# Optimization experiments

Measured on AMD Instinct MI355X. Metric: run time of the kernel, lower is better.

The kernel has to match this reference:

```python
import jax, jax.numpy as jnp
import numpy as np

EPS = 1e-3  # keras LayerNormalization default epsilon

def _ln(x, gamma, beta):
    m = jnp.mean(x, axis=-1, keepdims=True)
    v = jnp.var(x, axis=-1, keepdims=True)
    return gamma * (x - m) * jax.lax.rsqrt(v + EPS) + beta

def setup_inputs() -> dict:
    B, T, F, H = 256, 128, 4, 512  # T*F must equal H (skip-connection constraint in context GRN)
    D = T * F
    key = jax.random.key(0)
    ks = jax.random.split(key, 16)
    s = lambda fan: 1.0 / np.sqrt(fan)
    inp = {
        "inputs": jax.random.normal(ks[0], (B, T, F), jnp.float32),
        # context GRN (input dim D = T*F = H)
        "W1c": jax.random.normal(ks[1], (D, H), jnp.float32) * s(D),
        "b1c": jnp.zeros((H,), jnp.float32),
        "W2c": jax.random.normal(ks[2], (H, H), jnp.float32) * s(H),
        "b2c": jnp.zeros((H,), jnp.float32),
        "Wgc": jax.random.normal(ks[3], (H, H), jnp.float32) * s(H),
        "bgc": jnp.zeros((H,), jnp.float32),
        "gamma_c": jnp.ones((H,), jnp.float32),
        "beta_c": jnp.zeros((H,), jnp.float32),
        # softmax variable-selection head
        "Wsel": jax.random.normal(ks[4], (H, F), jnp.float32) * s(H),
        "bsel": jnp.zeros((F,), jnp.float32),
        # F per-variable GRNs, batched over leading F axis (input dim 1)
        "w1": jax.random.normal(ks[5], (F, H), jnp.float32),
        "b1": jnp.zeros((F, H), jnp.float32),
        "W2": jax.random.normal(ks[6], (F, H, H), jnp.float32) * s(H),
        "b2": jnp.zeros((F, H), jnp.float32),
        "Wg": jax.random.normal(ks[7], (F, H, H), jnp.float32) * s(H),
        "bg": jnp.zeros((F, H), jnp.float32),
        "gamma": jnp.ones((F, H), jnp.float32),
        "beta": jnp.zeros((F, H), jnp.float32),
    }
    return inp

def reference(inputs, W1c, b1c, W2c, b2c, Wgc, bgc, gamma_c, beta_c,
              Wsel, bsel, w1, b1, W2, b2, Wg, bg, gamma, beta):
    B, T, F = inputs.shape
    # ---- context GRN on flattened inputs (skip == flat since T*F == H) ----
    flat = inputs.reshape(B, T * F)
    x = jax.nn.elu(flat @ W1c + b1c)
    x = x @ W2c + b2c
    g = jax.nn.sigmoid(x @ Wgc + bgc)
    ctx = _ln(g * x + (1.0 - g) * flat, gamma_c, beta_c)
    # ---- softmax selection weights over variables ----
    sel = jax.nn.softmax(ctx @ Wsel + bsel)  # [B, F]
    # ---- per-variable GRNs, batched over F (input is scalar per variable) ----
    v = inputs[..., None]                              # [B,T,F,1] (skip path)
    x1 = jax.nn.elu(v * w1 + b1)                       # [B,T,F,H]
    x2 = jnp.einsum('btfh,fhk->btfk', x1, W2) + b2     # dense2
    gv = jax.nn.sigmoid(jnp.einsum('btfh,fhk->btfk', x2, Wg) + bg)
    gated = gv * x2 + (1.0 - gv) * v                   # skip broadcasts [B,T,F,1]
    tv = _ln(gated, gamma, beta)                       # [B,T,F,H]
    # ---- weighted sum over variables ----
    selected = jnp.einsum('btfh,bf->bth', tv, sel)     # [B,T,H]
    sel_weights = jnp.tile(sel[:, None, None, :], (1, T, 1, 1))  # [B,T,1,F]
    return selected, sel_weights
```

## Files before the change

kernel.cpp:

```cpp
#include <hip/hip_runtime.h>
#include <math.h>


#define H 512
#define NF 4
#define MTOT 32768

typedef unsigned short u16;
typedef unsigned int u32;
typedef __attribute__((ext_vector_type(8))) short short8;
typedef __attribute__((ext_vector_type(4))) float f32x4;
typedef __attribute__((ext_vector_type(4))) u32 u32x4;

__device__ __forceinline__ u16 f2bf(float x) {
  union { float f; u32 u; } v; v.f = x;
  return (u16)((v.u + 0x7fffu + ((v.u >> 16) & 1u)) >> 16);
}
__device__ __forceinline__ float bf2f(u32 h16) {
  union { u32 u; float f; } v; v.u = h16 << 16;
  return v.f;
}
__device__ __forceinline__ float elu_f(float x) {
  return x > 0.0f ? x : (__expf(x) - 1.0f);
}
__device__ __forceinline__ float sigmoid_f(float x) {
  return __builtin_amdgcn_rcpf(1.0f + __expf(-x));
}
__device__ __forceinline__ u32 cvtpk(float lo, float hi) {
  u32 r;
  asm("v_cvt_pk_bf16_f32 %0, %1, %2" : "=v"(r) : "v"(lo), "v"(hi));
  return r;
}
template <int CTRL>
__device__ __forceinline__ float dppadd(float v) {
  int t = __builtin_amdgcn_update_dpp(0, __float_as_int(v), CTRL, 0xF, 0xF, true);
  return v + __int_as_float(t);
}
__device__ __forceinline__ float red16(float v) {
  v = dppadd<0xB1>(v);
  v = dppadd<0x4E>(v);
  v = dppadd<0x141>(v);
  v = dppadd<0x140>(v);
  return v;
}

__device__ __forceinline__ void glld16(const void* g, void* l) {
  __builtin_amdgcn_global_load_lds(
      (const __attribute__((address_space(1))) u32*)(unsigned long long)(uintptr_t)g,
      (__attribute__((address_space(3))) u32*)(u32)(uintptr_t)l, 16, 0, 0);
}

#define MFMA16(a, b, c) __builtin_amdgcn_mfma_f32_16x16x32_bf16((a), (b), (c), 0, 0, 0)

__device__ __forceinline__ int sA_idx(int m, int n) {
  return m * 512 + ((((n >> 3) ^ (m & 7)) << 3) + (n & 7));
}

__device__ __forceinline__ void gridbar(u32* cnt, u32 target) {
  __syncthreads();
  __threadfence();
  if (threadIdx.x == 0) {
    __hip_atomic_fetch_add(cnt, 1u, __ATOMIC_RELEASE, __HIP_MEMORY_SCOPE_AGENT);
    while (__hip_atomic_load(cnt, __ATOMIC_ACQUIRE, __HIP_MEMORY_SCOPE_AGENT) < target)
      __builtin_amdgcn_s_sleep(8);
  }
  __syncthreads();
  __threadfence();
}

struct TileCtx {
  int tid, wid, lane, quad, col;
};

__global__ __launch_bounds__(256)
void pack_all(const float* __restrict__ W2, const float* __restrict__ Wg,
              const float* __restrict__ W1c, const float* __restrict__ W2c,
              const float* __restrict__ Wgc,
              u16* __restrict__ W2p, u16* __restrict__ Wgp, u16* __restrict__ Cp,
              u32* __restrict__ bar) {
  int g = blockIdx.x * 256 + threadIdx.x;
  if (g == 0) { bar[0] = 0; bar[1] = 0; }
  int r = g & 32767; int mat = g >> 15;
  if (mat >= 11) return;
  const float* src; u16* dst;
  if (mat < 4)      { src = W2 + (size_t)mat * 262144;       dst = W2p + (size_t)mat * 262144; }
  else if (mat < 8) { src = Wg + (size_t)(mat - 4) * 262144; dst = Wgp + (size_t)(mat - 4) * 262144; }
  else              { src = (mat == 8 ? W1c : (mat == 9 ? W2c : Wgc));
                      dst = Cp + (size_t)(mat - 8) * 262144; }
  dst += (size_t)r * 8;
  int lane = r & 63;
  int n, k0;
  if (mat == 8 || mat == 9) {
    int nb = r >> 12, kk = (r >> 8) & 15, ntg = (r >> 6) & 3;
    n  = nb * 64 + ntg * 16 + (lane & 15);
    k0 = kk * 32 + (lane >> 4) * 8;
  } else {
    int nt = (r >> 6) & 31, kk = (r >> 11) & 15;
    n  = nt * 16 + (lane & 15);
    k0 = kk * 32 + (lane >> 4) * 8;
  }
  short8 pk;
  #pragma unroll
  for (int j = 0; j < 8; ++j) pk[j] = (short)f2bf(src[(size_t)(k0 + j) * H + n]);
  *(short8*)dst = pk;
}

__device__ __forceinline__ void slab_kloop(const TileCtx& c, const u16* Wslab,
                                           u16* sA, u16* sB0, u16* sB1,
                                           f32x4 acc[4]) {
  #pragma unroll 1
  for (int kk = 0; kk < 16; ++kk) {
    if (kk < 15)
      glld16(Wslab + (kk + 1) * 2048 + c.tid * 8,
             (((kk + 1) & 1) ? sB1 : sB0) + c.tid * 8);
    const u16* bp = ((kk & 1) ? sB1 : sB0) + c.wid * 512 + c.lane * 8;
    short8 bb = *(const short8*)(bp);
    const int kq = kk * 4 + c.quad;
    const int s0 = (kq ^ (c.col & 7)) * 8;
    short8 a0 = *(const short8*)&sA[(     c.col) * 512 + s0];
    short8 a1 = *(const short8*)&sA[(16 + c.col) * 512 + s0];
    short8 a2 = *(const short8*)&sA[(32 + c.col) * 512 + s0];
    short8 a3 = *(const short8*)&sA[(48 + c.col) * 512 + s0];
    acc[0] = MFMA16(a0, bb, acc[0]);
    acc[1] = MFMA16(a1, bb, acc[1]);
    acc[2] = MFMA16(a2, bb, acc[2]);
    acc[3] = MFMA16(a3, bb, acc[3]);
    __syncthreads();
  }
}

__global__ __launch_bounds__(256)
void ctx_fused(const float* __restrict__ in, const u16* __restrict__ Cp,
               const float* __restrict__ b1c, const float* __restrict__ b2c,
               const float* __restrict__ bgc,
               const float* __restrict__ gamma_c, const float* __restrict__ beta_c,
               const float* __restrict__ Wsel, const float* __restrict__ bsel,
               u16* __restrict__ x1g, u16* __restrict__ xg,
               float* __restrict__ sel_ws, float* __restrict__ selw_out,
               u32* __restrict__ bar)
{
  __shared__ __align__(16) u16 smem[49152];
  TileCtx c;
  c.tid = threadIdx.x; c.wid = c.tid >> 6; c.lane = c.tid & 63;
  c.quad = c.lane >> 4; c.col = c.lane & 15;
  const int blk = blockIdx.x;
  const int mb = blk >> 3, nb = blk & 7;
  const int m0 = mb * 64;

  {
    u16* const sA  = smem;
    u16* const sB0 = smem + 32768;
    u16* const sB1 = smem + 34816;
    const u16* Wslab = Cp + (size_t)nb * 32768;
    glld16(Wslab + c.tid * 8, sB0 + c.tid * 8);
    {
      const int m = c.tid >> 2;
      const int kb = (c.tid & 3) * 128;
      const float* rowp = in + (size_t)(m0 + m) * H;
      #pragma unroll
      for (int gg = 0; gg < 16; ++gg) {
        const int ge = (gg + (c.tid & 3) * 4) & 15;
        const int k = kb + ge * 8;
        float4 v0 = *(const float4*)&rowp[k];
        float4 v1 = *(const float4*)&rowp[k + 4];
        u32x4 pk4;
        pk4.x = cvtpk(v0.x, v0.y); pk4.y = cvtpk(v0.z, v0.w);
        pk4.z = cvtpk(v1.x, v1.y); pk4.w = cvtpk(v1.z, v1.w);
        const int grp = (k >> 3) ^ (m & 7);
        *(u32x4*)&sA[m * 512 + grp * 8] = pk4;
      }
    }
    __syncthreads();
    f32x4 acc[4];
    #pragma unroll
    for (int mt = 0; mt < 4; ++mt) acc[mt] = (f32x4){0,0,0,0};
    slab_kloop(c, Wslab, sA, sB0, sB1, acc);
    const int n = nb * 64 + c.wid * 16 + c.col;
    const float bv = b1c[n];
    #pragma unroll
    for (int mt = 0; mt < 4; ++mt)
      #pragma unroll
      for (int reg = 0; reg < 4; ++reg) {
        const int m = m0 + mt * 16 + c.quad * 4 + reg;
        x1g[(size_t)m * H + n] = f2bf(elu_f(acc[mt][reg] + bv));
      }
  }
  gridbar(bar + 0, 32);

  {
    u16* const sA  = smem;
    u16* const sB0 = smem + 32768;
    u16* const sB1 = smem + 34816;
    const u16* Wslab = Cp + 262144 + (size_t)nb * 32768;
    glld16(Wslab + c.tid * 8, sB0 + c.tid * 8);
    {
      const int m = c.tid >> 2;
      const int kb = (c.tid & 3) * 128;
      const u16* rowp = x1g + (size_t)(m0 + m) * H;
      #pragma unroll
      for (int gg = 0; gg < 16; ++gg) {
        const int ge = (gg + (c.tid & 3) * 4) & 15;
        const int k = kb + ge * 8;
        short8 w = *(const short8*)&rowp[k];
        const int grp = (k >> 3) ^ (m & 7);
        *(short8*)&sA[m * 512 + grp * 8] = w;
      }
    }
    __syncthreads();
    f32x4 acc[4];
    #pragma unroll
    for (int mt = 0; mt < 4; ++mt) acc[mt] = (f32x4){0,0,0,0};
    slab_kloop(c, Wslab, sA, sB0, sB1, acc);
    const int n = nb * 64 + c.wid * 16 + c.col;
    const float bv = b2c[n];
    #pragma unroll
    for (int mt = 0; mt < 4; ++mt)
      #pragma unroll
      for (int reg = 0; reg < 4; ++reg) {
        const int m = m0 + mt * 16 + c.quad * 4 + reg;
        xg[(size_t)m * H + n] = f2bf(acc[mt][reg] + bv);
      }
  }
  gridbar(bar + 1, 32);
  if (blk >= 8) return;

  {
    u16* const sA  = smem;
    u16* const sB0 = smem + 16384;
    u16* const sB1 = smem + 32768;
    float* const sRedF = (float*)sB0;
    float* const sZp  = sRedF + 1024;
    float* const sZf  = sRedF + 1792;
    float* const sSel = sRedF + 1952;
    const int b0 = blk * 32;
    const u16* Wgcp = Cp + 524288;

    #pragma unroll
    for (int i = 0; i < 8; ++i)
      glld16(Wgcp + (i * 256 + c.tid) * 8, sB0 + (i * 256 + c.tid) * 8);

    {
      const int m  = c.tid >> 3;
      const int kb = (c.tid & 7) * 64;
      const u16* rowp = xg + (size_t)(b0 + m) * H;
      #pragma unroll
      for (int gg = 0; gg < 8; ++gg) {
        const int ge = (gg + (c.tid & 7)) & 7;
        const int k = kb + ge * 8;
        short8 w = *(const short8*)&rowp[k];
        const int grp = (k >> 3) ^ (m & 7);
        *(short8*)&sA[m * 512 + grp * 8] = w;
      }
    }
    __syncthreads();

    f32x4 acc[2][8];
    #pragma unroll
    for (int mt = 0; mt < 2; ++mt)
      #pragma unroll
      for (int j = 0; j < 8; ++j) acc[mt][j] = (f32x4){0,0,0,0};

    #pragma unroll 1
    for (int kk = 0; kk < 16; ++kk) {
      if (kk < 15) {
        const u16* src = Wgcp + (kk + 1) * 16384;
        u16* dst = ((kk + 1) & 1) ? sB1 : sB0;
        #pragma unroll
        for (int i = 0; i < 8; ++i)
          glld16(src + (i * 256 + c.tid) * 8, dst + (i * 256 + c.tid) * 8);
      }
      const u16* bp = (kk & 1) ? sB1 : sB0;
      short8 bb[8];
      #pragma unroll
      for (int j = 0; j < 8; ++j)
        bb[j] = *(const short8*)(bp + ((c.wid * 8 + j) * 64 + c.lane) * 8);
      const int kq = kk * 4 + c.quad;
      const int s0 = (kq ^ (c.col & 7)) * 8;
      short8 a0 = *(const short8*)&sA[(     c.col) * 512 + s0];
      short8 a1 = *(const short8*)&sA[(16 + c.col) * 512 + s0];
      #pragma unroll
      for (int j = 0; j < 8; ++j) acc[0][j] = MFMA16(a0, bb[j], acc[0][j]);
      #pragma unroll
      for (int j = 0; j < 8; ++j) acc[1][j] = MFMA16(a1, bb[j], acc[1][j]);
      __syncthreads();
    }

    {
      float bv[8];
      #pragma unroll
      for (int j = 0; j < 8; ++j) bv[j] = bgc[c.wid * 128 + j * 16 + c.col];
      #pragma unroll
      for (int mt = 0; mt < 2; ++mt)
        #pragma unroll
        for (int j = 0; j < 8; ++j) {
          const int n = c.wid * 128 + j * 16 + c.col;
          #pragma unroll
          for (int reg = 0; reg < 4; ++reg) {
            const int m = mt * 16 + c.quad * 4 + reg;
            const float xv = bf2f(sA[sA_idx(m, n)]);
            const float fl = in[(size_t)(b0 + m) * H + n];
            const float gv = sigmoid_f(acc[mt][j][reg] + bv[j]);
            acc[mt][j][reg] = gv * xv + (1.0f - gv) * fl;
          }
        }
    }

    #pragma unroll
    for (int mt = 0; mt < 2; ++mt) {
      float rs[4], rq[4];
      #pragma unroll
      for (int reg = 0; reg < 4; ++reg) {
        rs[reg] = 0.f; rq[reg] = 0.f;
        #pragma unroll
        for (int j = 0; j < 8; ++j) {
          const float gt = acc[mt][j][reg];
          rs[reg] += gt; rq[reg] += gt * gt;
        }
        rs[reg] = red16(rs[reg]);
        rq[reg] = red16(rq[reg]);
      }
      if (c.col == 0) {
        #pragma unroll
        for (int reg = 0; reg < 4; ++reg) {
          const int m = mt * 16 + c.quad * 4 + reg;
          float2 sq; sq.x = rs[reg]; sq.y = rq[reg];
          *(float2*)&sRedF[m * 20 + c.wid * 2] = sq;
        }
      }
    }
    __syncthreads();
    if (c.tid < 32) {
      const int row = c.tid;
      float s = 0.f, q = 0.f;
      #pragma unroll
      for (int jj = 0; jj < 2; ++jj) {
        float4 v = *(float4*)&sRedF[row * 20 + jj * 4];
        s += v.x + v.z; q += v.y + v.w;
      }
      const float mu = s * (1.0f / H);
      const float rstd = rsqrtf(q * (1.0f / H) - mu * mu + 1e-3f);
      float2 mr; mr.x = mu; mr.y = rstd;
      *(float2*)&sRedF[640 + row * 2] = mr;
    }
    __syncthreads();

    {
      float gm[8], bt[8]; float4 ws4[8];
      #pragma unroll
      for (int j = 0; j < 8; ++j) {
        const int n = c.wid * 128 + j * 16 + c.col;
        gm[j] = gamma_c[n]; bt[j] = beta_c[n];
        ws4[j] = *(const float4*)&Wsel[n * NF];
      }
      #pragma unroll
      for (int mt = 0; mt < 2; ++mt)
        #pragma unroll
        for (int reg = 0; reg < 4; ++reg) {
          const int m = mt * 16 + c.quad * 4 + reg;
          float2 mr = *(float2*)&sRedF[640 + m * 2];
          float zp[4] = {0.f, 0.f, 0.f, 0.f};
          #pragma unroll
          for (int j = 0; j < 8; ++j) {
            const float ctxv = gm[j] * ((acc[mt][j][reg] - mr.x) * mr.y) + bt[j];
            zp[0] = fmaf(ctxv, ws4[j].x, zp[0]);
            zp[1] = fmaf(ctxv, ws4[j].y, zp[1]);
            zp[2] = fmaf(ctxv, ws4[j].z, zp[2]);
            zp[3] = fmaf(ctxv, ws4[j].w, zp[3]);
          }
          #pragma unroll
          for (int f = 0; f < 4; ++f) zp[f] = red16(zp[f]);
          if (c.col == 0) {
            #pragma unroll
            for (int f = 0; f < 4; ++f) sZp[(m * 4 + c.wid) * 4 + f] = zp[f];
          }
        }
    }
    __syncthreads();
    if (c.tid < 128) {
      const int m = c.tid >> 2, f = c.tid & 3;
      float z = bsel[f];
      #pragma unroll
      for (int w = 0; w < 4; ++w) z += sZp[(m * 4 + w) * 4 + f];
      sZf[m * 4 + f] = z;
    }
    __syncthreads();
    if (c.tid < 32) {
      const int m = c.tid;
      float z0 = sZf[m*4], z1 = sZf[m*4+1], z2 = sZf[m*4+2], z3 = sZf[m*4+3];
      float mx = fmaxf(fmaxf(z0, z1), fmaxf(z2, z3));
      float e0 = __expf(z0-mx), e1 = __expf(z1-mx), e2 = __expf(z2-mx), e3 = __expf(z3-mx);
      float inv = __builtin_amdgcn_rcpf(e0 + e1 + e2 + e3);
      sSel[m*4]   = e0*inv; sSel[m*4+1] = e1*inv;
      sSel[m*4+2] = e2*inv; sSel[m*4+3] = e3*inv;
      sel_ws[(b0+m)*NF]   = e0*inv; sel_ws[(b0+m)*NF+1] = e1*inv;
      sel_ws[(b0+m)*NF+2] = e2*inv; sel_ws[(b0+m)*NF+3] = e3*inv;
    }
    __syncthreads();
    {
      const int m = c.tid >> 3;
      const int jb = (c.tid & 7) * 64;
      float4 v; v.x = sSel[m*4]; v.y = sSel[m*4+1]; v.z = sSel[m*4+2]; v.w = sSel[m*4+3];
      #pragma unroll
      for (int j = 0; j < 16; ++j)
        *(float4*)&selw_out[(size_t)(b0 + m) * H + jb + j * 4] = v;
    }
  }
}


__device__ __forceinline__ void stage_chunk8(int tid, const u16* src, u16* dst) {
  glld16(src + tid * 8,         dst + tid * 8);
  glld16(src + tid * 8 + 4096,  dst + tid * 8 + 4096);
  glld16(src + tid * 8 + 8192,  dst + tid * 8 + 8192);
  glld16(src + tid * 8 + 12288, dst + tid * 8 + 12288);
}

template <bool PREFETCH_TAIL>
__device__ __forceinline__ void gemm_kloop8(const TileCtx& c, const u16* Wp,
                                            const u16* nextWp,
                                            u16* sA, u16* sB0, u16* sB1,
                                            f32x4 acc[4][4]) {
  #pragma unroll 1
  for (int kk = 0; kk < 16; ++kk) {
    if (kk < 15) {
      stage_chunk8(c.tid, Wp + (kk + 1) * 16384, (((kk + 1) & 1) ? sB1 : sB0));
    } else if (PREFETCH_TAIL) {
      stage_chunk8(c.tid, nextWp, sB0);
    }
    const u16* bp = ((kk & 1) ? sB1 : sB0) + c.wid * 2048 + c.lane * 8;
    short8 bb[4];
    #pragma unroll
    for (int nt = 0; nt < 4; ++nt) bb[nt] = *(const short8*)(bp + nt * 512);
    const int kq = kk * 4 + c.quad;
    const int s0 = (kq ^ (c.col & 7)) * 8;
    #pragma unroll
    for (int mt = 0; mt < 4; ++mt) {
      short8 a = *(const short8*)&sA[(mt * 16 + c.col) * 512 + s0];
      #pragma unroll
      for (int nt = 0; nt < 4; ++nt)
        acc[mt][nt] = MFMA16(a, bb[nt], acc[mt][nt]);
    }
    __syncthreads();
  }
}

__device__ __forceinline__ void store_x2_pair_n(const TileCtx& c, u16* sA,
                                                int mt, int n, u32 o01, u32 o23) {
  const bool even = (c.lane & 1) == 0;
  const u32 send = even ? o23 : o01;
  const u32 recv = (u32)__builtin_amdgcn_update_dpp(0, (int)send, 0xB1, 0xF, 0xF, true);
  const u32 hi = even ? recv : o23;
  const u32 lo = even ? o01 : recv;
  const u32 dlo = __builtin_amdgcn_perm(hi, lo, 0x05040100u);
  const u32 dhi = __builtin_amdgcn_perm(hi, lo, 0x07060302u);
  const int np = n & ~1;
  const int mA = mt * 16 + c.quad * 4 + (even ? 0 : 2);
  const int iA = mA * 512 + ((((np >> 3) ^ (mA & 7)) << 3) + (np & 7));
  const int mB = mA + 1;
  const int iB = mB * 512 + ((((np >> 3) ^ (mB & 7)) << 3) + (np & 7));
  *(u32*)&sA[iA] = dlo;
  *(u32*)&sA[iB] = dhi;
}

__device__ __forceinline__ void ln_reduce8(const TileCtx& c, float* sRedF,
                                           f32x4 acc[4][4]) {
  #pragma unroll
  for (int mt = 0; mt < 4; ++mt) {
    float rs[4], rq[4];
    #pragma unroll
    for (int reg = 0; reg < 4; ++reg) {
      rs[reg] = 0.f; rq[reg] = 0.f;
      #pragma unroll
      for (int nt = 0; nt < 4; ++nt) {
        const float gt = acc[mt][nt][reg];
        rs[reg] += gt; rq[reg] += gt * gt;
      }
      rs[reg] = red16(rs[reg]);
      rq[reg] = red16(rq[reg]);
    }
    if (c.col == 0) {
      #pragma unroll
      for (int reg = 0; reg < 4; ++reg) {
        const int m = mt * 16 + c.quad * 4 + reg;
        float2 sq; sq.x = rs[reg]; sq.y = rq[reg];
        *(float2*)&sRedF[m * 20 + c.wid * 2] = sq;
      }
    }
  }
  __syncthreads();
  if (c.tid < 64) {
    const int row = c.tid;
    float s = 0.f, q = 0.f;
    #pragma unroll
    for (int jj = 0; jj < 4; ++jj) {
      float4 v = *(float4*)&sRedF[row * 20 + jj * 4];
      s += v.x + v.z; q += v.y + v.w;
    }
    const float mu = s * (1.0f / H);
    const float rstd = rsqrtf(q * (1.0f / H) - mu * mu + 1e-3f);
    float2 mr; mr.x = mu; mr.y = rstd;
    *(float2*)&sRedF[1280 + row * 2] = mr;
  }
  __syncthreads();
}

__global__ __launch_bounds__(512, 2)
void vsn_mfma(const float* __restrict__ in,
              const float* __restrict__ w1, const float* __restrict__ b1,
              const float* __restrict__ b2, const float* __restrict__ bg,
              const float* __restrict__ gamma, const float* __restrict__ beta,
              const u16* __restrict__ W2p, const u16* __restrict__ Wgp,
              const float* __restrict__ sel_ws,
              float* __restrict__ out)
{
  __shared__ __align__(16) u16 smem[65536];
  u16* const sA  = smem;
  u16* const sB0 = smem + 32768;
  u16* const sB1 = smem + 49152;
  float* const sRedF = (float*)smem;

  TileCtx c;
  c.tid = threadIdx.x; c.wid = c.tid >> 6; c.lane = c.tid & 63;
  c.quad = c.lane >> 4; c.col = c.lane & 15;
  const int row0 = blockIdx.x * 64;
  const int bidx = row0 >> 7;

  f32x4 outacc[4][4];
  #pragma unroll
  for (int mt = 0; mt < 4; ++mt)
    #pragma unroll
    for (int nt = 0; nt < 4; ++nt) outacc[mt][nt] = (f32x4){0,0,0,0};

  stage_chunk8(c.tid, W2p, sB0);

  #pragma unroll 1
  for (int f = 0; f < NF; ++f) {
    const u16* W2f = W2p + (size_t)f * 262144;
    const u16* Wgf = Wgp + (size_t)f * 262144;
    const u16* W2n = W2p + (size_t)((f + 1) & 3) * 262144;

    {
      const int m  = c.tid >> 3;
      const int kb = (c.tid & 7) * 64;
      const float v = in[(size_t)(row0 + m) * NF + f];
      const float* w1f = w1 + f * H;
      const float* b1f = b1 + f * H;
      #pragma unroll
      for (int gg = 0; gg < 8; ++gg) {
        const int ge = (gg + (c.tid & 7)) & 7;
        const int k = kb + ge * 8;
        float4 wv0 = *(const float4*)&w1f[k];
        float4 wv1 = *(const float4*)&w1f[k + 4];
        float4 bv0 = *(const float4*)&b1f[k];
        float4 bv1 = *(const float4*)&b1f[k + 4];
        u32x4 pk4;
        pk4.x = cvtpk(elu_f(fmaf(v, wv0.x, bv0.x)), elu_f(fmaf(v, wv0.y, bv0.y)));
        pk4.y = cvtpk(elu_f(fmaf(v, wv0.z, bv0.z)), elu_f(fmaf(v, wv0.w, bv0.w)));
        pk4.z = cvtpk(elu_f(fmaf(v, wv1.x, bv1.x)), elu_f(fmaf(v, wv1.y, bv1.y)));
        pk4.w = cvtpk(elu_f(fmaf(v, wv1.z, bv1.z)), elu_f(fmaf(v, wv1.w, bv1.w)));
        const int grp = (k >> 3) ^ (m & 7);
        *(u32x4*)&sA[m * 512 + grp * 8] = pk4;
      }
    }
    __syncthreads();

    f32x4 acc[4][4];
    #pragma unroll
    for (int mt = 0; mt < 4; ++mt)
      #pragma unroll
      for (int nt = 0; nt < 4; ++nt) acc[mt][nt] = (f32x4){0,0,0,0};

    gemm_kloop8<true>(c, W2f, Wgf, sA, sB0, sB1, acc);

    u32 x2p[4][4][2];
    {
      float bv[4];
      #pragma unroll
      for (int nt = 0; nt < 4; ++nt) bv[nt] = b2[f * H + c.wid * 64 + nt * 16 + c.col];
      #pragma unroll
      for (int mt = 0; mt < 4; ++mt)
        #pragma unroll
        for (int nt = 0; nt < 4; ++nt) {
          const u32 o01 = cvtpk(acc[mt][nt][0] + bv[nt], acc[mt][nt][1] + bv[nt]);
          const u32 o23 = cvtpk(acc[mt][nt][2] + bv[nt], acc[mt][nt][3] + bv[nt]);
          x2p[mt][nt][0] = o01; x2p[mt][nt][1] = o23;
          store_x2_pair_n(c, sA, mt, c.wid * 64 + nt * 16 + c.col, o01, o23);
        }
    }
    __syncthreads();

    #pragma unroll
    for (int mt = 0; mt < 4; ++mt)
      #pragma unroll
      for (int nt = 0; nt < 4; ++nt) acc[mt][nt] = (f32x4){0,0,0,0};
    gemm_kloop8<true>(c, Wgf, W2n, sA, sB0, sB1, acc);

    {
      const float selw = sel_ws[bidx * NF + f];
      float bv[4];
      #pragma unroll
      for (int nt = 0; nt < 4; ++nt) bv[nt] = bg[f * H + c.wid * 64 + nt * 16 + c.col];
      #pragma unroll
      for (int mt = 0; mt < 4; ++mt) {
        float vr[4];
        #pragma unroll
        for (int reg = 0; reg < 4; ++reg)
          vr[reg] = in[(size_t)(row0 + mt * 16 + c.quad * 4 + reg) * NF + f];
        #pragma unroll
        for (int nt = 0; nt < 4; ++nt)
          #pragma unroll
          for (int reg = 0; reg < 4; ++reg) {
            const u32 w = x2p[mt][nt][reg >> 1];
            const float x2v = bf2f((reg & 1) ? (w >> 16) : (w & 0xffffu));
            const float gv = sigmoid_f(acc[mt][nt][reg] + bv[nt]);
            acc[mt][nt][reg] = gv * x2v + (1.0f - gv) * vr[reg];
          }
      }
      ln_reduce8(c, sRedF, acc);
      float gm[4], bt[4];
      #pragma unroll
      for (int nt = 0; nt < 4; ++nt) {
        const int n = f * H + c.wid * 64 + nt * 16 + c.col;
        gm[nt] = gamma[n]; bt[nt] = beta[n];
      }
      #pragma unroll
      for (int mt = 0; mt < 4; ++mt)
        #pragma unroll
        for (int reg = 0; reg < 4; ++reg) {
          const int m = mt * 16 + c.quad * 4 + reg;
          float2 mr = *(float2*)&sRedF[1280 + m * 2];
          #pragma unroll
          for (int nt = 0; nt < 4; ++nt) {
            const float tv = gm[nt] * ((acc[mt][nt][reg] - mr.x) * mr.y) + bt[nt];
            outacc[mt][nt][reg] = fmaf(selw, tv, outacc[mt][nt][reg]);
          }
        }
      __syncthreads();
    }
  }

  #pragma unroll
  for (int mt = 0; mt < 4; ++mt)
    #pragma unroll
    for (int reg = 0; reg < 4; ++reg) {
      const int m = row0 + mt * 16 + c.quad * 4 + reg;
      #pragma unroll
      for (int nt = 0; nt < 4; ++nt)
        out[(size_t)m * H + c.wid * 64 + nt * 16 + c.col] = outacc[mt][nt][reg];
    }
}

extern "C" void kernel_launch(void* const* d_in, const int* in_sizes, int n_in,
                              void* d_out, int out_size, void* d_ws, size_t ws_size,
                              hipStream_t stream) {
  const float* in_     = (const float*)d_in[0];
  const float* W1c     = (const float*)d_in[1];
  const float* b1c     = (const float*)d_in[2];
  const float* W2c     = (const float*)d_in[3];
  const float* b2c     = (const float*)d_in[4];
  const float* Wgc     = (const float*)d_in[5];
  const float* bgc     = (const float*)d_in[6];
  const float* gamma_c = (const float*)d_in[7];
  const float* beta_c  = (const float*)d_in[8];
  const float* Wsel    = (const float*)d_in[9];
  const float* bsel    = (const float*)d_in[10];
  const float* w1      = (const float*)d_in[11];
  const float* b1v     = (const float*)d_in[12];
  const float* W2      = (const float*)d_in[13];
  const float* b2v     = (const float*)d_in[14];
  const float* Wg      = (const float*)d_in[15];
  const float* bgv     = (const float*)d_in[16];
  const float* gma     = (const float*)d_in[17];
  const float* bta     = (const float*)d_in[18];

  float* out_sel = (float*)d_out;
  float* out_w   = (float*)d_out + (size_t)MTOT * H;

  float* sel_ws = (float*)d_ws;
  u16*   W2p    = (u16*)((char*)d_ws + 4096);
  u16*   Wgp    = W2p + (size_t)NF * H * H;
  u16*   Cp     = Wgp + (size_t)NF * H * H;
  u16*   x1g    = Cp + 3 * 262144;
  u16*   xg     = x1g + 131072;
  u32*   bar    = (u32*)(xg + 131072);

  hipLaunchKernelGGL(pack_all, dim3(1408), dim3(256), 0, stream,
                     W2, Wg, W1c, W2c, Wgc, W2p, Wgp, Cp, bar);
  hipLaunchKernelGGL(ctx_fused, dim3(32), dim3(256), 0, stream,
                     in_, Cp, b1c, b2c, bgc, gamma_c, beta_c, Wsel, bsel,
                     x1g, xg, sel_ws, out_w, bar);
  hipLaunchKernelGGL(vsn_mfma, dim3(MTOT / 64), dim3(512), 0, stream,
                     in_, w1, b1v, b2v, bgv, gma, bta, W2p, Wgp, sel_ws, out_sel);
}
```

Baseline: 427.7 us.

## Make B-tile staging per-wave to remove block barriers from GEMM k-loop

Each wave now stages only its own slice of the weight chunk into a private double-buffered LDS region. The k-loop can then wait on its own vmcnt instead of a block-wide __syncthreads each iteration. MFMA sections are wrapped in s_setprio to favour issue. Prefetch of the next GEMM's weights moves to explicit points, with added barriers around the LN reduction. This trades block-level sync for hand-placed waitcnt, which relies on glld16 emitting exactly the expected number of vm ops and on LDS-direct loads being complete when vmcnt drops.

```diff
diff --git a/kernel.cpp b/kernel.cpp
--- a/kernel.cpp
+++ b/kernel.cpp
@@ -408,31 +408,34 @@
 }
 
 
-__device__ __forceinline__ void stage_chunk8(int tid, const u16* src, u16* dst) {
-  glld16(src + tid * 8,         dst + tid * 8);
-  glld16(src + tid * 8 + 4096,  dst + tid * 8 + 4096);
-  glld16(src + tid * 8 + 8192,  dst + tid * 8 + 8192);
-  glld16(src + tid * 8 + 12288, dst + tid * 8 + 12288);
-}
-
-template <bool PREFETCH_TAIL>
-__device__ __forceinline__ void gemm_kloop8(const TileCtx& c, const u16* Wp,
-                                            const u16* nextWp,
-                                            u16* sA, u16* sB0, u16* sB1,
-                                            f32x4 acc[4][4]) {
+__device__ __forceinline__ void stage_slice(int wid, int lane, const u16* chunk, u16* dstbuf) {
+  const u16* src = chunk + wid * 2048 + lane * 8;
+  u16* dst = dstbuf + lane * 8;
+  glld16(src,        dst);
+  glld16(src + 512,  dst + 512);
+  glld16(src + 1024, dst + 1024);
+  glld16(src + 1536, dst + 1536);
+}
+
+__device__ __forceinline__ void gemm_kloop_nb(const TileCtx& c, const u16* Wp,
+                                              const u16* sA, u16* sBw,
+                                              f32x4 acc[4][4]) {
   #pragma unroll 1
   for (int kk = 0; kk < 16; ++kk) {
     if (kk < 15) {
-      stage_chunk8(c.tid, Wp + (kk + 1) * 16384, (((kk + 1) & 1) ? sB1 : sB0));
-    } else if (PREFETCH_TAIL) {
-      stage_chunk8(c.tid, nextWp, sB0);
-    }
-    const u16* bp = ((kk & 1) ? sB1 : sB0) + c.wid * 2048 + c.lane * 8;
+      stage_slice(c.wid, c.lane, Wp + (kk + 1) * 16384, sBw + ((kk + 1) & 1) * 2048);
+      asm volatile("s_waitcnt vmcnt(4)" ::: "memory");
+    } else {
+      asm volatile("s_waitcnt vmcnt(0)" ::: "memory");
+    }
+    __builtin_amdgcn_sched_barrier(0);
+    const u16* bp = sBw + (kk & 1) * 2048 + c.lane * 8;
     short8 bb[4];
     #pragma unroll
     for (int nt = 0; nt < 4; ++nt) bb[nt] = *(const short8*)(bp + nt * 512);
     const int kq = kk * 4 + c.quad;
     const int s0 = (kq ^ (c.col & 7)) * 8;
+    __builtin_amdgcn_s_setprio(1);
     #pragma unroll
     for (int mt = 0; mt < 4; ++mt) {
       short8 a = *(const short8*)&sA[(mt * 16 + c.col) * 512 + s0];
@@ -440,7 +443,7 @@
       for (int nt = 0; nt < 4; ++nt)
         acc[mt][nt] = MFMA16(a, bb[nt], acc[mt][nt]);
     }
-    __syncthreads();
+    __builtin_amdgcn_s_setprio(0);
   }
 }
 
@@ -515,13 +518,13 @@
 {
   __shared__ __align__(16) u16 smem[65536];
   u16* const sA  = smem;
-  u16* const sB0 = smem + 32768;
-  u16* const sB1 = smem + 49152;
+  u16* const sB  = smem + 32768;
   float* const sRedF = (float*)smem;
 
   TileCtx c;
   c.tid = threadIdx.x; c.wid = c.tid >> 6; c.lane = c.tid & 63;
   c.quad = c.lane >> 4; c.col = c.lane & 15;
+  u16* const sBw = sB + c.wid * 4096;
   const int row0 = blockIdx.x * 64;
   const int bidx = row0 >> 7;
 
@@ -531,13 +534,12 @@
     #pragma unroll
     for (int nt = 0; nt < 4; ++nt) outacc[mt][nt] = (f32x4){0,0,0,0};
 
-  stage_chunk8(c.tid, W2p, sB0);
+  stage_slice(c.wid, c.lane, W2p, sBw);
 
   #pragma unroll 1
   for (int f = 0; f < NF; ++f) {
     const u16* W2f = W2p + (size_t)f * 262144;
     const u16* Wgf = Wgp + (size_t)f * 262144;
-    const u16* W2n = W2p + (size_t)((f + 1) & 3) * 262144;
 
     {
       const int m  = c.tid >> 3;
@@ -570,7 +572,10 @@
       #pragma unroll
       for (int nt = 0; nt < 4; ++nt) acc[mt][nt] = (f32x4){0,0,0,0};
 
-    gemm_kloop8<true>(c, W2f, Wgf, sA, sB0, sB1, acc);
+    gemm_kloop_nb(c, W2f, sA, sBw, acc);
+    __syncthreads();
+
+    stage_slice(c.wid, c.lane, Wgf, sBw);
 
     u32 x2p[4][4][2];
     {
@@ -593,7 +598,7 @@
     for (int mt = 0; mt < 4; ++mt)
       #pragma unroll
       for (int nt = 0; nt < 4; ++nt) acc[mt][nt] = (f32x4){0,0,0,0};
-    gemm_kloop8<true>(c, Wgf, W2n, sA, sB0, sB1, acc);
+    gemm_kloop_nb(c, Wgf, sA, sBw, acc);
 
     {
       const float selw = sel_ws[bidx * NF + f];
@@ -616,6 +621,7 @@
             acc[mt][nt][reg] = gv * x2v + (1.0f - gv) * vr[reg];
           }
       }
+      __syncthreads();
       ln_reduce8(c, sRedF, acc);
       float gm[4], bt[4];
       #pragma unroll
@@ -635,6 +641,8 @@
             outacc[mt][nt][reg] = fmaf(selw, tv, outacc[mt][nt][reg]);
           }
         }
+      if (f < NF - 1)
+        stage_slice(c.wid, c.lane, W2p + (size_t)(f + 1) * 262144, sBw);
       __syncthreads();
     }
   }
```

After: 369.9 us. 13.5% less time.

## Load GEMM weight fragments directly into registers instead of LDS staging

Applied to the files above, without the earlier changes.

Each wave now reads its B-operand fragments straight from global memory into a register double buffer, prefetching the next k-step (and the next matrix's first step) while issuing MFMAs. This removes the LDS staging buffers and the barrier after every k-step. The dense2 output goes to a separate LDS tile that the gate epilogue reads back, instead of being held in registers. MFMA sections are wrapped in s_setprio. The risk is that global-load latency is covered by only one k-step of prefetch, and per-wave global reads may be less coalesced than the old cooperative staging.

```diff
diff --git a/kernel.cpp b/kernel.cpp
--- a/kernel.cpp
+++ b/kernel.cpp
@@ -408,43 +408,41 @@
 }
 
 
-__device__ __forceinline__ void stage_chunk8(int tid, const u16* src, u16* dst) {
-  glld16(src + tid * 8,         dst + tid * 8);
-  glld16(src + tid * 8 + 4096,  dst + tid * 8 + 4096);
-  glld16(src + tid * 8 + 8192,  dst + tid * 8 + 8192);
-  glld16(src + tid * 8 + 12288, dst + tid * 8 + 12288);
-}
-
-template <bool PREFETCH_TAIL>
-__device__ __forceinline__ void gemm_kloop8(const TileCtx& c, const u16* Wp,
-                                            const u16* nextWp,
-                                            u16* sA, u16* sB0, u16* sB1,
-                                            f32x4 acc[4][4]) {
+__device__ __forceinline__ void mfma_step(const TileCtx& c, const u16* sAsrc,
+                                          int kk, const short8 bb[4],
+                                          f32x4 acc[4][4]) {
+  const int kq = kk * 4 + c.quad;
+  const int s0 = (kq ^ (c.col & 7)) * 8;
+  __builtin_amdgcn_s_setprio(1);
+  #pragma unroll
+  for (int mt = 0; mt < 4; ++mt) {
+    short8 a = *(const short8*)&sAsrc[(mt * 16 + c.col) * 512 + s0];
+    #pragma unroll
+    for (int nt = 0; nt < 4; ++nt)
+      acc[mt][nt] = MFMA16(a, bb[nt], acc[mt][nt]);
+  }
+  __builtin_amdgcn_s_setprio(0);
+}
+
+__device__ __forceinline__ void gemm_kloop_reg(const TileCtx& c, const u16* Wp,
+                                               const u16* Wnext, const u16* sAsrc,
+                                               short8 b0[4], f32x4 acc[4][4]) {
+  const int off = c.wid * 2048 + c.lane * 8;
+  short8 b1[4];
   #pragma unroll 1
-  for (int kk = 0; kk < 16; ++kk) {
-    if (kk < 15) {
-      stage_chunk8(c.tid, Wp + (kk + 1) * 16384, (((kk + 1) & 1) ? sB1 : sB0));
-    } else if (PREFETCH_TAIL) {
-      stage_chunk8(c.tid, nextWp, sB0);
-    }
-    const u16* bp = ((kk & 1) ? sB1 : sB0) + c.wid * 2048 + c.lane * 8;
-    short8 bb[4];
-    #pragma unroll
-    for (int nt = 0; nt < 4; ++nt) bb[nt] = *(const short8*)(bp + nt * 512);
-    const int kq = kk * 4 + c.quad;
-    const int s0 = (kq ^ (c.col & 7)) * 8;
-    #pragma unroll
-    for (int mt = 0; mt < 4; ++mt) {
-      short8 a = *(const short8*)&sA[(mt * 16 + c.col) * 512 + s0];
-      #pragma unroll
-      for (int nt = 0; nt < 4; ++nt)
-        acc[mt][nt] = MFMA16(a, bb[nt], acc[mt][nt]);
-    }
-    __syncthreads();
-  }
-}
-
-__device__ __forceinline__ void store_x2_pair_n(const TileCtx& c, u16* sA,
+  for (int kk = 0; kk < 16; kk += 2) {
+    const u16* s1 = Wp + (kk + 1) * 16384 + off;
+    #pragma unroll
+    for (int nt = 0; nt < 4; ++nt) b1[nt] = *(const short8*)(s1 + nt * 512);
+    mfma_step(c, sAsrc, kk, b0, acc);
+    const u16* s2 = (kk < 14) ? (Wp + (kk + 2) * 16384 + off) : (Wnext + off);
+    #pragma unroll
+    for (int nt = 0; nt < 4; ++nt) b0[nt] = *(const short8*)(s2 + nt * 512);
+    mfma_step(c, sAsrc, kk + 1, b1, acc);
+  }
+}
+
+__device__ __forceinline__ void store_x2_pair_n(const TileCtx& c, u16* dstT,
                                                 int mt, int n, u32 o01, u32 o23) {
   const bool even = (c.lane & 1) == 0;
   const u32 send = even ? o23 : o01;
@@ -458,8 +456,8 @@
   const int iA = mA * 512 + ((((np >> 3) ^ (mA & 7)) << 3) + (np & 7));
   const int mB = mA + 1;
   const int iB = mB * 512 + ((((np >> 3) ^ (mB & 7)) << 3) + (np & 7));
-  *(u32*)&sA[iA] = dlo;
-  *(u32*)&sA[iB] = dhi;
+  *(u32*)&dstT[iA] = dlo;
+  *(u32*)&dstT[iB] = dhi;
 }
 
 __device__ __forceinline__ void ln_reduce8(const TileCtx& c, float* sRedF,
@@ -514,9 +512,8 @@
               float* __restrict__ out)
 {
   __shared__ __align__(16) u16 smem[65536];
-  u16* const sA  = smem;
-  u16* const sB0 = smem + 32768;
-  u16* const sB1 = smem + 49152;
+  u16* const sA = smem;
+  u16* const sX = smem + 32768;
   float* const sRedF = (float*)smem;
 
   TileCtx c;
@@ -531,7 +528,12 @@
     #pragma unroll
     for (int nt = 0; nt < 4; ++nt) outacc[mt][nt] = (f32x4){0,0,0,0};
 
-  stage_chunk8(c.tid, W2p, sB0);
+  short8 b0[4];
+  {
+    const u16* s = W2p + c.wid * 2048 + c.lane * 8;
+    #pragma unroll
+    for (int nt = 0; nt < 4; ++nt) b0[nt] = *(const short8*)(s + nt * 512);
+  }
 
   #pragma unroll 1
   for (int f = 0; f < NF; ++f) {
@@ -570,9 +572,8 @@
       #pragma unroll
       for (int nt = 0; nt < 4; ++nt) acc[mt][nt] = (f32x4){0,0,0,0};
 
-    gemm_kloop8<true>(c, W2f, Wgf, sA, sB0, sB1, acc);
-
-    u32 x2p[4][4][2];
+    gemm_kloop_reg(c, W2f, Wgf, sA, b0, acc);
+
     {
       float bv[4];
       #pragma unroll
@@ -583,8 +584,7 @@
         for (int nt = 0; nt < 4; ++nt) {
           const u32 o01 = cvtpk(acc[mt][nt][0] + bv[nt], acc[mt][nt][1] + bv[nt]);
           const u32 o23 = cvtpk(acc[mt][nt][2] + bv[nt], acc[mt][nt][3] + bv[nt]);
-          x2p[mt][nt][0] = o01; x2p[mt][nt][1] = o23;
-          store_x2_pair_n(c, sA, mt, c.wid * 64 + nt * 16 + c.col, o01, o23);
+          store_x2_pair_n(c, sX, mt, c.wid * 64 + nt * 16 + c.col, o01, o23);
         }
     }
     __syncthreads();
@@ -593,7 +593,7 @@
     for (int mt = 0; mt < 4; ++mt)
       #pragma unroll
       for (int nt = 0; nt < 4; ++nt) acc[mt][nt] = (f32x4){0,0,0,0};
-    gemm_kloop8<true>(c, Wgf, W2n, sA, sB0, sB1, acc);
+    gemm_kloop_reg(c, Wgf, W2n, sX, b0, acc);
 
     {
       const float selw = sel_ws[bidx * NF + f];
@@ -607,14 +607,16 @@
         for (int reg = 0; reg < 4; ++reg)
           vr[reg] = in[(size_t)(row0 + mt * 16 + c.quad * 4 + reg) * NF + f];
         #pragma unroll
-        for (int nt = 0; nt < 4; ++nt)
+        for (int nt = 0; nt < 4; ++nt) {
+          const int n = c.wid * 64 + nt * 16 + c.col;
           #pragma unroll
           for (int reg = 0; reg < 4; ++reg) {
-            const u32 w = x2p[mt][nt][reg >> 1];
-            const float x2v = bf2f((reg & 1) ? (w >> 16) : (w & 0xffffu));
+            const int m = mt * 16 + c.quad * 4 + reg;
+            const float x2v = bf2f(sX[sA_idx(m, n)]);
             const float gv = sigmoid_f(acc[mt][nt][reg] + bv[nt]);
             acc[mt][nt][reg] = gv * x2v + (1.0f - gv) * vr[reg];
           }
+        }
       }
       ln_reduce8(c, sRedF, acc);
       float gm[4], bt[4];
```

Result: slower. 519.0 us (+21.3%).
